# Kernel optimization log

Measured on AMD Instinct MI355X. Metric: run time of the kernel, lower is better.

## Reference

```python
import jax, jax.numpy as jnp
import numpy as np

B, D, Q, K, C = 1024, 256, 131072, 200, 1000
TEMPERATURE = 0.07  # train-mode temperature (test=False path)
EPS = 1e-05


def setup_inputs() -> dict:
    key = jax.random.key(0)
    k1, k2, k3 = jax.random.split(key, 3)
    x = jax.random.normal(k1, (B, D), dtype=jnp.float32)
    memory = jax.random.normal(k2, (Q, D), dtype=jnp.float32)
    memory_label = jax.random.randint(k3, (Q,), 0, C, dtype=jnp.int64 if jax.config.jax_enable_x64 else jnp.int32)
    return {"x": x, "memory": memory, "memory_label": memory_label}


def reference(x, memory, memory_label):
    # dist = normalize(x) @ memory.T  -> [B, Q]
    xn = x / jnp.linalg.norm(x, axis=-1, keepdims=True)
    dist = jnp.einsum('bd,qd->bq', xn, memory)
    # top-k similarities and indices -> [B, K]
    sim_weight, sim_indices = jax.lax.top_k(dist, K)
    sim_labels = memory_label[sim_indices]  # [B, K]
    w = jax.nn.softmax(sim_weight / TEMPERATURE, axis=1)  # [B, K]
    # Fused one-hot scatter + weighted sum: scatter-add weights per class.
    rows = jnp.arange(B)[:, None]  # [B, 1] broadcast against [B, K]
    pred_scores = jnp.zeros((B, C), dtype=w.dtype).at[rows, sim_labels].add(w)
    return jnp.minimum(pred_scores + EPS, 1.0)
```

## Files before the change

kernel.cpp:

```cpp
#include <hip/hip_runtime.h>
#include <hip/hip_bf16.h>
#include <hip/hip_fp16.h>

#define B_ 1024
#define D_ 256
#define Q_ 131072
#define K_ 200
#define C_ 1000
#define INV_T 14.285714285714286f
#define EPS_ 1e-5f
#define CAP 2048
#define T0S 43.2f

#define TBM 256
#define SBN 32
#define CS 16
#define HCAP 1024
#define FT 512

typedef __attribute__((ext_vector_type(2))) long lng2;
typedef __attribute__((ext_vector_type(4))) float f32x4;

__device__ __forceinline__ unsigned key_of(float v) {
    unsigned u = __float_as_uint(v);
    return (u & 0x80000000u) ? ~u : (u | 0x80000000u);
}
__device__ __forceinline__ int binof(float v) {
    int b = (int)(key_of(v) >> 16) - 0xC000;
    return b < 0 ? 0 : (b > 255 ? 255 : b);
}
__device__ __forceinline__ unsigned pk4(float a, float b, float c, float d) {
    int u = __builtin_amdgcn_cvt_pk_fp8_f32(a, b, 0, false);
    u = __builtin_amdgcn_cvt_pk_fp8_f32(c, d, u, true);
    return (unsigned)u;
}

#define MFMA_FP8 __builtin_amdgcn_mfma_f32_16x16x32_fp8_fp8

__global__ __launch_bounds__(256) void normsplit_kernel(const float* __restrict__ x,
                                                        float* __restrict__ xn,
                                                        unsigned char* __restrict__ af8,
                                                        unsigned* __restrict__ cnt) {
    int row = blockIdx.x, tid = threadIdx.x;
    if (tid == 0) cnt[row] = 0u;
    float v = x[row * D_ + tid];
    float s = v * v;
#pragma unroll
    for (int off = 32; off > 0; off >>= 1) s += __shfl_xor(s, off);
    __shared__ float wsum[4];
    int lane = tid & 63, wid = tid >> 6;
    if (lane == 0) wsum[wid] = s;
    __syncthreads();
    float tot = wsum[0] + wsum[1] + wsum[2] + wsum[3];
    float xv = v / sqrtf(tot);
    xn[row * D_ + tid] = xv;
    int t = tid >> 5, kb = (tid >> 3) & 3, j = tid & 7;
    int p = __builtin_amdgcn_cvt_pk_fp8_f32(xv * 16.f, 0.f, 0, false);
    af8[row * 256 + kb * 64 + t * 8 + j] = (unsigned char)(p & 0xFF);
}

__global__ __launch_bounds__(256) void convB_kernel(const float* __restrict__ m,
                                                    uint4* __restrict__ bf8,
                                                    __half* __restrict__ mh) {
    const int NCH = Q_ * D_ / 16;
    for (int g = blockIdx.x * 256 + threadIdx.x; g < NCH; g += gridDim.x * 256) {
        int panel = g >> 9, o = g & 511;
        int P = o >> 7, r = o & 127, ch = r >> 6, w = r & 63, kb = w >> 4, c = w & 15;
        int q = panel * 32 + ch * 16 + c;
        const float* src = m + (size_t)q * D_ + P * 64 + kb * 8;
        float4 f0 = *(const float4*)(src);
        float4 f1 = *(const float4*)(src + 4);
        float4 g0 = *(const float4*)(src + 32);
        float4 g1 = *(const float4*)(src + 36);
        uint4 ov;
        ov.x = pk4(f0.x, f0.y, f0.z, f0.w);
        ov.y = pk4(f1.x, f1.y, f1.z, f1.w);
        ov.z = pk4(g0.x, g0.y, g0.z, g0.w);
        ov.w = pk4(g1.x, g1.y, g1.z, g1.w);
        bf8[g] = ov;
        __half* mhp = mh + (size_t)q * D_ + P * 64 + kb * 8;
        __half2 ph[4];
        ph[0] = __floats2half2_rn(f0.x, f0.y); ph[1] = __floats2half2_rn(f0.z, f0.w);
        ph[2] = __floats2half2_rn(f1.x, f1.y); ph[3] = __floats2half2_rn(f1.z, f1.w);
        *(uint4*)mhp = *(const uint4*)ph;
        ph[0] = __floats2half2_rn(g0.x, g0.y); ph[1] = __floats2half2_rn(g0.z, g0.w);
        ph[2] = __floats2half2_rn(g1.x, g1.y); ph[3] = __floats2half2_rn(g1.z, g1.w);
        *(uint4*)(mhp + 32) = *(const uint4*)ph;
    }
}

__global__ __launch_bounds__(512, 4) void mfma_gemm_filter(const unsigned char* __restrict__ Af8,
                                                           const unsigned char* __restrict__ Bf8,
                                                           unsigned* __restrict__ candi,
                                                           unsigned* __restrict__ cnt) {
    __shared__ unsigned hits[HCAP];
    __shared__ unsigned hcnt;

    const int tid = threadIdx.x;
    const int lane = tid & 63, wid = tid >> 6;
    const int l15 = lane & 15, kb = lane >> 4;

    const int l = blockIdx.x;
    const int logical = (l & 7) * 128 + (l >> 3);
    const int colgroup = logical >> 2;
    const int band = logical & 3;
    const int arow0 = band * TBM;

    if (tid == 0) hcnt = 0u;
    __syncthreads();

    long a[2][8];
#pragma unroll
    for (int m = 0; m < 2; ++m) {
        const unsigned char* ab = Af8 + (size_t)(arow0 + wid * 32 + m * 16 + l15) * 256 + kb * 64;
#pragma unroll
        for (int t2 = 0; t2 < 4; ++t2) {
            lng2 v = *(const lng2*)(ab + t2 * 16);
            a[m][2 * t2] = v.x;
            a[m][2 * t2 + 1] = v.y;
        }
    }

    const unsigned char* Bwave = Bf8 + (size_t)colgroup * (CS * 8192) + (((kb << 4) + l15) << 4);
#define LDB(CS_, P_, N_) (*(const lng2*)(Bwave + (size_t)(CS_) * 8192 + (P_) * 2048 + (N_) * 1024))

    f32x4 zero4 = {0.f, 0.f, 0.f, 0.f};
    f32x4 acc[2][2];
#pragma unroll
    for (int m = 0; m < 2; ++m)
#pragma unroll
        for (int n = 0; n < 2; ++n) acc[m][n] = zero4;

#define MFMA8(B0, B1, P_) do {                                                 \
    acc[0][0] = MFMA_FP8(a[0][2 * (P_)], (B0).x, acc[0][0], 0, 0, 0);          \
    acc[1][0] = MFMA_FP8(a[1][2 * (P_)], (B0).x, acc[1][0], 0, 0, 0);          \
    acc[0][1] = MFMA_FP8(a[0][2 * (P_)], (B1).x, acc[0][1], 0, 0, 0);          \
    acc[1][1] = MFMA_FP8(a[1][2 * (P_)], (B1).x, acc[1][1], 0, 0, 0);          \
    acc[0][0] = MFMA_FP8(a[0][2 * (P_) + 1], (B0).y, acc[0][0], 0, 0, 0);      \
    acc[1][0] = MFMA_FP8(a[1][2 * (P_) + 1], (B0).y, acc[1][0], 0, 0, 0);      \
    acc[0][1] = MFMA_FP8(a[0][2 * (P_) + 1], (B1).y, acc[0][1], 0, 0, 0);      \
    acc[1][1] = MFMA_FP8(a[1][2 * (P_) + 1], (B1).y, acc[1][1], 0, 0, 0);      \
} while (0)

#define LOADPANEL(BUF, CS_) do {                                               \
    _Pragma("unroll")                                                          \
    for (int P_ = 0; P_ < 4; ++P_) {                                           \
        BUF[P_][0] = LDB(CS_, P_, 0);                                          \
        BUF[P_][1] = LDB(CS_, P_, 1);                                          \
    }                                                                          \
} while (0)

#define COMPPANEL(BUF) do {                                                    \
    _Pragma("unroll")                                                          \
    for (int P_ = 0; P_ < 4; ++P_) MFMA8(BUF[P_][0], BUF[P_][1], P_);          \
} while (0)

#define FILTER(CS_) do {                                                       \
    _Pragma("unroll")                                                          \
    for (int m = 0; m < 2; ++m)                                                \
        _Pragma("unroll")                                                      \
        for (int n = 0; n < 2; ++n) {                                          \
            float mx_ = fmaxf(fmaxf(acc[m][n][0], acc[m][n][1]),               \
                              fmaxf(acc[m][n][2], acc[m][n][3]));              \
            if (mx_ > T0S) {                                                   \
                const unsigned gc_ = (unsigned)(colgroup * (CS * SBN) + (CS_) * SBN + n * 16 + l15); \
                _Pragma("unroll")                                              \
                for (int r = 0; r < 4; ++r) {                                  \
                    if (acc[m][n][r] > T0S) {                                  \
                        unsigned lr_ = (unsigned)(wid * 32 + m * 16 + kb * 4 + r); \
                        unsigned p_ = atomicAdd(&hcnt, 1u);                    \
                        if (p_ < HCAP) hits[p_] = (lr_ << 17) | gc_;           \
                    }                                                          \
                }                                                              \
            }                                                                  \
            acc[m][n] = zero4;                                                 \
        }                                                                      \
} while (0)

    lng2 bufA[4][2], bufB[4][2];
    LOADPANEL(bufA, 0);
#pragma unroll 1
    for (int cs2 = 0; cs2 < CS; cs2 += 2) {
        LOADPANEL(bufB, cs2 + 1);
        COMPPANEL(bufA);
        FILTER(cs2);
        if (cs2 + 2 < CS) LOADPANEL(bufA, cs2 + 2);
        COMPPANEL(bufB);
        FILTER(cs2 + 1);
    }

    __syncthreads();
    const unsigned nh = (hcnt < (unsigned)HCAP) ? hcnt : (unsigned)HCAP;
    for (unsigned i = tid; i < nh; i += 512) {
        unsigned e = hits[i];
        int grow = band * TBM + (int)(e >> 17);
        unsigned gcol = e & 0x1FFFFu;
        unsigned pos = atomicAdd(&cnt[grow], 1u);
        if (pos < CAP) candi[(long long)grow * CAP + pos] = gcol;
    }
#undef LDB
#undef MFMA8
#undef LOADPANEL
#undef COMPPANEL
#undef FILTER
}

__global__ __launch_bounds__(FT) void final_kernel(const unsigned* __restrict__ cnt,
                                                   const unsigned* __restrict__ candi,
                                                   const float* __restrict__ xn,
                                                   const __half* __restrict__ mh,
                                                   const int* __restrict__ labels,
                                                   float* __restrict__ out) {
    __shared__ float cval[CAP];
    __shared__ unsigned cidx[CAP];
    __shared__ unsigned char incl[CAP];
    __shared__ float xs[D_];
    __shared__ float bins[C_];
    __shared__ float segf[FT];
    __shared__ unsigned hist[256];
    __shared__ float binval[256];
    __shared__ int binpos[256];
    __shared__ int sh_bstar, sh_g0, sh_m;

    const int tid = threadIdx.x;
    const int row = blockIdx.x;
    unsigned c = cnt[row];
    const int n = (c < (unsigned)CAP) ? (int)c : CAP;

    if (tid < D_) xs[tid] = xn[row * D_ + tid];
    for (int i = tid; i < C_; i += FT) bins[i] = 0.f;
    if (tid < 256) hist[tid] = 0u;
    if (tid == 0) sh_m = 0;
    for (int i = tid; i < n; i += FT) cidx[i] = candi[(long long)row * CAP + i];
    __syncthreads();

    for (int i = tid; i < n; i += FT) {
        const uint4* mrow = (const uint4*)(mh + (size_t)cidx[i] * D_);
        float s = 0.f;
#pragma unroll 8
        for (int k = 0; k < 32; ++k) {
            uint4 mv = mrow[k];
            const __half2* hp = (const __half2*)&mv;
            float2 f0 = __half22float2(hp[0]);
            float2 f1 = __half22float2(hp[1]);
            float2 f2 = __half22float2(hp[2]);
            float2 f3 = __half22float2(hp[3]);
            const float* xp = xs + k * 8;
            s += f0.x * xp[0] + f0.y * xp[1] + f1.x * xp[2] + f1.y * xp[3]
               + f2.x * xp[4] + f2.y * xp[5] + f3.x * xp[6] + f3.y * xp[7];
        }
        cval[i] = s;
    }
    __syncthreads();

    float lm = -3.4e38f;
    for (int i = tid; i < n; i += FT) lm = fmaxf(lm, cval[i]);
    segf[tid] = lm;
    __syncthreads();
    for (int off = FT / 2; off > 0; off >>= 1) {
        if (tid < off) segf[tid] = fmaxf(segf[tid], segf[tid + off]);
        __syncthreads();
    }
    const float m = segf[0];
    __syncthreads();

    if (n > K_) {
        for (int i = tid; i < n; i += FT) atomicAdd(&hist[binof(cval[i])], 1u);
        __syncthreads();
        if (tid == 0) {
            unsigned cum = 0; int b = 255;
            for (; b >= 0; --b) { cum += hist[b]; if (cum >= (unsigned)K_) break; }
            sh_bstar = b;
            sh_g0 = (int)(cum - hist[b]);
        }
        __syncthreads();
        const int bst = sh_bstar;
        for (int i = tid; i < n; i += FT) {
            int hb = binof(cval[i]);
            incl[i] = (hb > bst) ? (unsigned char)1 : (unsigned char)0;
            if (hb == bst) {
                int p = atomicAdd(&sh_m, 1);
                if (p < 256) { binval[p] = cval[i]; binpos[p] = i; }
            }
        }
        __syncthreads();
        const int m2 = (sh_m < 256) ? sh_m : 256;
        const int rem = K_ - sh_g0;
        for (int e = tid; e < m2; e += FT) {
            unsigned ke = key_of(binval[e]);
            int g = 0;
            for (int j = 0; j < m2; ++j) {
                unsigned kj = key_of(binval[j]);
                g += (kj > ke) || (kj == ke && j < e);
            }
            incl[binpos[e]] = (g < rem) ? (unsigned char)1 : (unsigned char)0;
        }
        __syncthreads();
    } else {
        for (int i = tid; i < n; i += FT) incl[i] = 1;
        __syncthreads();
    }

    float part = 0.f;
    for (int i = tid; i < n; i += FT) {
        float e = incl[i] ? __expf((cval[i] - m) * INV_T) : 0.f;
        cval[i] = e;
        part += e;
    }
    segf[tid] = part;
    __syncthreads();
    for (int off = FT / 2; off > 0; off >>= 1) {
        if (tid < off) segf[tid] += segf[tid + off];
        __syncthreads();
    }
    const float invS = 1.f / segf[0];

    for (int i = tid; i < n; i += FT) {
        float e = cval[i];
        if (e > 0.f) {
            int lbl = labels[cidx[i]];
            if ((unsigned)lbl < (unsigned)C_) atomicAdd(&bins[lbl], e);
        }
    }
    __syncthreads();

    const long long ob = (long long)row * C_;
    for (int i = tid; i < C_; i += FT)
        out[ob + i] = fminf(bins[i] * invS + EPS_, 1.0f);
}

extern "C" void kernel_launch(void* const* d_in, const int* in_sizes, int n_in,
                              void* d_out, int out_size, void* d_ws, size_t ws_size,
                              hipStream_t stream) {
    const float* x = (const float*)d_in[0];
    const float* mem = (const float*)d_in[1];
    const int* lab = (const int*)d_in[2];
    float* out = (float*)d_out;

    float* xn = (float*)d_ws;
    unsigned char* Af8 = (unsigned char*)(xn + (size_t)B_ * D_);
    unsigned char* Bf8 = Af8 + (size_t)B_ * D_;
    __half* mh = (__half*)(Bf8 + (size_t)Q_ * D_);
    unsigned* candi = (unsigned*)(mh + (size_t)Q_ * D_);
    unsigned* cnt = candi + (size_t)B_ * CAP;

    normsplit_kernel<<<B_, 256, 0, stream>>>(x, xn, Af8, cnt);
    convB_kernel<<<4096, 256, 0, stream>>>(mem, (uint4*)Bf8, mh);
    mfma_gemm_filter<<<(B_ / TBM) * (Q_ / (SBN * CS)), 512, 0, stream>>>(Af8, Bf8, candi, cnt);
    final_kernel<<<B_, FT, 0, stream>>>(cnt, candi, xn, mh, lab, out);
}
```

Baseline: 190.6 us.

## Retile FP8 GEMM-filter: 128-row bands, 2x4 wave grid, 64-row per-wave A tiles

Changes the work split of the fused FP8 GEMM + threshold filter kernel. Each block now covers 128 rows by 1024 columns, arranged as a 2x4 grid of waves. Each wave keeps a 64-row A fragment in registers and streams one 16-column B slice per step, where it previously held 32 rows and two 16-column slices. The intent is more A reuse per B load and fewer B bytes per wave, at the cost of more A registers and more blocks that each load B.

```diff
diff --git a/kernel.cpp b/kernel.cpp
--- a/kernel.cpp
+++ b/kernel.cpp
@@ -12,9 +12,8 @@
 #define CAP 2048
 #define T0S 43.2f
 
-#define TBM 256
-#define SBN 32
-#define CS 16
+#define TBM 128
+#define NSL 16
 #define HCAP 1024
 #define FT 512
 
@@ -98,21 +97,22 @@
 
     const int tid = threadIdx.x;
     const int lane = tid & 63, wid = tid >> 6;
+    const int wr = wid >> 2, wn = wid & 3;
     const int l15 = lane & 15, kb = lane >> 4;
 
     const int l = blockIdx.x;
     const int logical = (l & 7) * 128 + (l >> 3);
-    const int colgroup = logical >> 2;
-    const int band = logical & 3;
+    const int cg = logical >> 3;
+    const int band = logical & 7;
     const int arow0 = band * TBM;
 
     if (tid == 0) hcnt = 0u;
     __syncthreads();
 
-    long a[2][8];
+    long a[4][8];
 #pragma unroll
-    for (int m = 0; m < 2; ++m) {
-        const unsigned char* ab = Af8 + (size_t)(arow0 + wid * 32 + m * 16 + l15) * 256 + kb * 64;
+    for (int m = 0; m < 4; ++m) {
+        const unsigned char* ab = Af8 + (size_t)(arow0 + wr * 64 + m * 16 + l15) * 256 + kb * 64;
 #pragma unroll
         for (int t2 = 0; t2 < 4; ++t2) {
             lng2 v = *(const lng2*)(ab + t2 * 16);
@@ -121,72 +121,64 @@
         }
     }
 
-    const unsigned char* Bwave = Bf8 + (size_t)colgroup * (CS * 8192) + (((kb << 4) + l15) << 4);
-#define LDB(CS_, P_, N_) (*(const lng2*)(Bwave + (size_t)(CS_) * 8192 + (P_) * 2048 + (N_) * 1024))
+    const unsigned char* Bwave = Bf8 + (size_t)cg * 262144 + (wn >> 1) * 8192
+                               + (wn & 1) * 1024 + (((kb << 4) + l15) << 4);
+#define LDB(I_, P_) (*(const lng2*)(Bwave + (size_t)(I_) * 16384 + (P_) * 2048))
 
     f32x4 zero4 = {0.f, 0.f, 0.f, 0.f};
-    f32x4 acc[2][2];
+    f32x4 acc[4];
 #pragma unroll
-    for (int m = 0; m < 2; ++m)
-#pragma unroll
-        for (int n = 0; n < 2; ++n) acc[m][n] = zero4;
-
-#define MFMA8(B0, B1, P_) do {                                                 \
-    acc[0][0] = MFMA_FP8(a[0][2 * (P_)], (B0).x, acc[0][0], 0, 0, 0);          \
-    acc[1][0] = MFMA_FP8(a[1][2 * (P_)], (B0).x, acc[1][0], 0, 0, 0);          \
-    acc[0][1] = MFMA_FP8(a[0][2 * (P_)], (B1).x, acc[0][1], 0, 0, 0);          \
-    acc[1][1] = MFMA_FP8(a[1][2 * (P_)], (B1).x, acc[1][1], 0, 0, 0);          \
-    acc[0][0] = MFMA_FP8(a[0][2 * (P_) + 1], (B0).y, acc[0][0], 0, 0, 0);      \
-    acc[1][0] = MFMA_FP8(a[1][2 * (P_) + 1], (B0).y, acc[1][0], 0, 0, 0);      \
-    acc[0][1] = MFMA_FP8(a[0][2 * (P_) + 1], (B1).y, acc[0][1], 0, 0, 0);      \
-    acc[1][1] = MFMA_FP8(a[1][2 * (P_) + 1], (B1).y, acc[1][1], 0, 0, 0);      \
+    for (int m = 0; m < 4; ++m) acc[m] = zero4;
+
+#define LOADSL(BUF, I_) do {                                                   \
+    _Pragma("unroll")                                                          \
+    for (int P_ = 0; P_ < 4; ++P_) BUF[P_] = LDB(I_, P_);                      \
 } while (0)
 
-#define LOADPANEL(BUF, CS_) do {                                               \
+#define COMPSL(BUF) do {                                                       \
     _Pragma("unroll")                                                          \
     for (int P_ = 0; P_ < 4; ++P_) {                                           \
-        BUF[P_][0] = LDB(CS_, P_, 0);                                          \
-        BUF[P_][1] = LDB(CS_, P_, 1);                                          \
+        acc[0] = MFMA_FP8(a[0][2 * P_], BUF[P_].x, acc[0], 0, 0, 0);           \
+        acc[1] = MFMA_FP8(a[1][2 * P_], BUF[P_].x, acc[1], 0, 0, 0);           \
+        acc[2] = MFMA_FP8(a[2][2 * P_], BUF[P_].x, acc[2], 0, 0, 0);           \
+        acc[3] = MFMA_FP8(a[3][2 * P_], BUF[P_].x, acc[3], 0, 0, 0);           \
+        acc[0] = MFMA_FP8(a[0][2 * P_ + 1], BUF[P_].y, acc[0], 0, 0, 0);       \
+        acc[1] = MFMA_FP8(a[1][2 * P_ + 1], BUF[P_].y, acc[1], 0, 0, 0);       \
+        acc[2] = MFMA_FP8(a[2][2 * P_ + 1], BUF[P_].y, acc[2], 0, 0, 0);       \
+        acc[3] = MFMA_FP8(a[3][2 * P_ + 1], BUF[P_].y, acc[3], 0, 0, 0);       \
     }                                                                          \
 } while (0)
 
-#define COMPPANEL(BUF) do {                                                    \
+#define FILTER(I_) do {                                                        \
+    const unsigned gc_ = (unsigned)(cg * 1024 + (wn + 4 * (I_)) * 16 + l15);   \
     _Pragma("unroll")                                                          \
-    for (int P_ = 0; P_ < 4; ++P_) MFMA8(BUF[P_][0], BUF[P_][1], P_);          \
-} while (0)
-
-#define FILTER(CS_) do {                                                       \
-    _Pragma("unroll")                                                          \
-    for (int m = 0; m < 2; ++m)                                                \
-        _Pragma("unroll")                                                      \
-        for (int n = 0; n < 2; ++n) {                                          \
-            float mx_ = fmaxf(fmaxf(acc[m][n][0], acc[m][n][1]),               \
-                              fmaxf(acc[m][n][2], acc[m][n][3]));              \
-            if (mx_ > T0S) {                                                   \
-                const unsigned gc_ = (unsigned)(colgroup * (CS * SBN) + (CS_) * SBN + n * 16 + l15); \
-                _Pragma("unroll")                                              \
-                for (int r = 0; r < 4; ++r) {                                  \
-                    if (acc[m][n][r] > T0S) {                                  \
-                        unsigned lr_ = (unsigned)(wid * 32 + m * 16 + kb * 4 + r); \
-                        unsigned p_ = atomicAdd(&hcnt, 1u);                    \
-                        if (p_ < HCAP) hits[p_] = (lr_ << 17) | gc_;           \
-                    }                                                          \
+    for (int m = 0; m < 4; ++m) {                                              \
+        float mx_ = fmaxf(fmaxf(acc[m][0], acc[m][1]),                         \
+                          fmaxf(acc[m][2], acc[m][3]));                        \
+        if (mx_ > T0S) {                                                       \
+            _Pragma("unroll")                                                  \
+            for (int r = 0; r < 4; ++r) {                                      \
+                if (acc[m][r] > T0S) {                                         \
+                    unsigned lr_ = (unsigned)(wr * 64 + m * 16 + kb * 4 + r);  \
+                    unsigned p_ = atomicAdd(&hcnt, 1u);                        \
+                    if (p_ < HCAP) hits[p_] = (lr_ << 17) | gc_;               \
                 }                                                              \
             }                                                                  \
-            acc[m][n] = zero4;                                                 \
         }                                                                      \
+        acc[m] = zero4;                                                        \
+    }                                                                          \
 } while (0)
 
-    lng2 bufA[4][2], bufB[4][2];
-    LOADPANEL(bufA, 0);
+    lng2 bufA[4], bufB[4];
+    LOADSL(bufA, 0);
 #pragma unroll 1
-    for (int cs2 = 0; cs2 < CS; cs2 += 2) {
-        LOADPANEL(bufB, cs2 + 1);
-        COMPPANEL(bufA);
-        FILTER(cs2);
-        if (cs2 + 2 < CS) LOADPANEL(bufA, cs2 + 2);
-        COMPPANEL(bufB);
-        FILTER(cs2 + 1);
+    for (int i2 = 0; i2 < NSL; i2 += 2) {
+        LOADSL(bufB, i2 + 1);
+        COMPSL(bufA);
+        FILTER(i2);
+        if (i2 + 2 < NSL) LOADSL(bufA, i2 + 2);
+        COMPSL(bufB);
+        FILTER(i2 + 1);
     }
 
     __syncthreads();
@@ -199,9 +191,8 @@
         if (pos < CAP) candi[(long long)grow * CAP + pos] = gcol;
     }
 #undef LDB
-#undef MFMA8
-#undef LOADPANEL
-#undef COMPPANEL
+#undef LOADSL
+#undef COMPSL
 #undef FILTER
 }
 
@@ -346,6 +337,6 @@
 
     normsplit_kernel<<<B_, 256, 0, stream>>>(x, xn, Af8, cnt);
     convB_kernel<<<4096, 256, 0, stream>>>(mem, (uint4*)Bf8, mh);
-    mfma_gemm_filter<<<(B_ / TBM) * (Q_ / (SBN * CS)), 512, 0, stream>>>(Af8, Bf8, candi, cnt);
+    mfma_gemm_filter<<<(B_ / TBM) * (Q_ / (NSL * 4 * 16)), 512, 0, stream>>>(Af8, Bf8, candi, cnt);
     final_kernel<<<B_, FT, 0, stream>>>(cnt, candi, xn, mh, lab, out);
 }
```

Result: no change. 190.8 us (+0.1%).
